# Kernel tuning notes

Hardware: AMD Instinct MI355X
Metric: run time of the kernel (lower is better)

## Reference

```python
import jax, jax.numpy as jnp
import numpy as np

BATCH = 50000      # number of target nodes in the batch (len(to_neighs))
DEGREE = 32        # fixed sampled neighbor count per node
NUM_NODES = 500000 # embedding table size (id2feat domain)
D_FEAT = 128       # feature dim of id2feat


def setup_inputs() -> dict:
    key = jax.random.key(0)
    k1, k2 = jax.random.split(key)
    neighs = jax.random.randint(k1, (BATCH, DEGREE), 0, NUM_NODES, dtype=jnp.int64)
    id2feat_table = jax.random.normal(k2, (NUM_NODES, D_FEAT), dtype=jnp.float32) * 0.02
    return {"neighs": neighs, "id2feat_table": id2feat_table}


def reference(neighs, id2feat_table):
    # Original: mask counts each neighbor occurrence, row-normalized by num_neigh,
    # then mask @ embed_matrix == per-node mean of neighbor embeddings.
    # Fixed degree K, so segment-mean == gather + mean over the neighbor axis.
    neigh_feats = id2feat_table[neighs]        # [B, K, D] gather (memory-bound)
    to_feats = neigh_feats.mean(axis=1)        # [B, D] mean over K neighbors
    return to_feats
```

## Files before the change

kernel.cpp:

```cpp
#include <hip/hip_runtime.h>


constexpr int BATCH  = 50000;
constexpr int DEGREE = 32;
constexpr int D_FEAT = 128;

typedef float f32x4 __attribute__((ext_vector_type(4)));

__global__ __launch_bounds__(256) void MeanAggregator_841813590039_kernel(
    const int* __restrict__ neighs,
    const float* __restrict__ table,
    float* __restrict__ out)
{
    const int wave  = (blockIdx.x * 256 + threadIdx.x) >> 6;
    const int lane  = threadIdx.x & 63;
    const int nodeA = wave * 2;
    const int col   = lane & 31;
    const int half  = lane & 32;

    const int rows = neighs[(size_t)nodeA * DEGREE + lane];

    #define ROW(k) __shfl(rows, half + (k), 64)
    #define LOADK(k) \
        reinterpret_cast<const f32x4*>(table + (size_t)ROW(k) * D_FEAT)[col]

    f32x4 buf0[8], buf1[8];

    #pragma unroll
    for (int j = 0; j < 8; ++j) buf0[j] = LOADK(j);

    f32x4 acc = {0.f, 0.f, 0.f, 0.f};

    #pragma unroll
    for (int g = 0; g < 3; ++g) {
        f32x4* cur = (g & 1) ? buf1 : buf0;
        f32x4* nxt = (g & 1) ? buf0 : buf1;
        #pragma unroll
        for (int j = 0; j < 8; ++j) nxt[j] = LOADK((g + 1) * 8 + j);
        #pragma unroll
        for (int j = 0; j < 8; ++j) acc += cur[j];
    }
    #pragma unroll
    for (int j = 0; j < 8; ++j) acc += buf1[j];

    #undef LOADK
    #undef ROW

    const float inv = 1.0f / (float)DEGREE;
    acc *= inv;

    const int node = nodeA + (half >> 5);
    f32x4* o = reinterpret_cast<f32x4*>(out + (size_t)node * D_FEAT) + col;
    __builtin_nontemporal_store(acc, o);
}

extern "C" void kernel_launch(void* const* d_in, const int* in_sizes, int n_in,
                              void* d_out, int out_size, void* d_ws, size_t ws_size,
                              hipStream_t stream) {
    const int*   neighs = (const int*)d_in[0];
    const float* table  = (const float*)d_in[1];
    float*       out    = (float*)d_out;

    const int grid = BATCH / 8;
    MeanAggregator_841813590039_kernel<<<grid, 256, 0, stream>>>(neighs, table, out);
}
```

Measured before the change: 400.6 us.

## Process eight node pairs per wave with bitonic-sorted neighbor ids

Each wave now handles eight node pairs instead of one, interleaving gathers across pairs with a double-buffered loop over the 32 neighbors. Neighbor ids for each node are bitonic-sorted within the 32-lane half before gathering, so loads issued together touch nearby table rows and may get better cache or TLB locality. The grid shrinks by a factor of eight, and launch bounds are raised to request higher occupancy. The costs are extra shuffle and compare work for the sort, higher register pressure from eight accumulators and buffers, and fewer waves available to hide latency.

```diff
diff --git a/kernel.cpp b/kernel.cpp
--- a/kernel.cpp
+++ b/kernel.cpp
@@ -4,54 +4,87 @@
 constexpr int BATCH  = 50000;
 constexpr int DEGREE = 32;
 constexpr int D_FEAT = 128;
+constexpr int PW     = 8;
+constexpr int NPAIRS = BATCH / 2;
+constexpr int WAVES  = (NPAIRS + PW - 1) / PW;
+constexpr int BLOCKS = (WAVES + 3) / 4;
 
 typedef float f32x4 __attribute__((ext_vector_type(4)));
 
-__global__ __launch_bounds__(256) void MeanAggregator_841813590039_kernel(
+__global__ __launch_bounds__(256, 4) void MeanAggregator_841813590039_kernel(
     const int* __restrict__ neighs,
     const float* __restrict__ table,
     float* __restrict__ out)
 {
-    const int wave  = (blockIdx.x * 256 + threadIdx.x) >> 6;
-    const int lane  = threadIdx.x & 63;
-    const int nodeA = wave * 2;
-    const int col   = lane & 31;
-    const int half  = lane & 32;
+    const int wave = blockIdx.x * 4 + (threadIdx.x >> 6);
+    const int lane = threadIdx.x & 63;
+    const int col  = lane & 31;
+    const int half = lane & 32;
 
-    const int rows = neighs[(size_t)nodeA * DEGREE + lane];
+    if (wave >= WAVES) return;
 
-    #define ROW(k) __shfl(rows, half + (k), 64)
-    #define LOADK(k) \
-        reinterpret_cast<const f32x4*>(table + (size_t)ROW(k) * D_FEAT)[col]
+    const int pair0 = wave * PW;
 
-    f32x4 buf0[8], buf1[8];
+    int rows[PW];
+    #pragma unroll
+    for (int i = 0; i < PW; ++i)
+        rows[i] = neighs[(size_t)(pair0 + i) * (2 * DEGREE) + lane];
 
     #pragma unroll
-    for (int j = 0; j < 8; ++j) buf0[j] = LOADK(j);
+    for (int i = 0; i < PW; ++i) {
+        int v = rows[i];
+        #pragma unroll
+        for (int size = 2; size <= 32; size <<= 1) {
+            #pragma unroll
+            for (int stride = size >> 1; stride > 0; stride >>= 1) {
+                const int  pv    = __shfl_xor(v, stride, 64);
+                const bool up    = ((col & size) == 0);
+                const bool lower = ((col & stride) == 0);
+                const int  mn    = (v < pv) ? v : pv;
+                const int  mx    = (v < pv) ? pv : v;
+                v = (lower == up) ? mn : mx;
+            }
+        }
+        rows[i] = v;
+    }
 
-    f32x4 acc = {0.f, 0.f, 0.f, 0.f};
+    #define LOADKJ(j, k) \
+        reinterpret_cast<const f32x4*>( \
+            table + (size_t)__shfl(rows[(j)], half + (k), 64) * D_FEAT)[col]
+
+    f32x4 acc[PW];
+    #pragma unroll
+    for (int j = 0; j < PW; ++j) acc[j] = f32x4{0.f, 0.f, 0.f, 0.f};
+
+    f32x4 buf0[PW], buf1[PW];
 
     #pragma unroll
-    for (int g = 0; g < 3; ++g) {
-        f32x4* cur = (g & 1) ? buf1 : buf0;
-        f32x4* nxt = (g & 1) ? buf0 : buf1;
+    for (int j = 0; j < PW; ++j) buf0[j] = LOADKJ(j, 0);
+
+    #pragma unroll
+    for (int k = 0; k < DEGREE - 1; ++k) {
+        f32x4* cur = (k & 1) ? buf1 : buf0;
+        f32x4* nxt = (k & 1) ? buf0 : buf1;
         #pragma unroll
-        for (int j = 0; j < 8; ++j) nxt[j] = LOADK((g + 1) * 8 + j);
+        for (int j = 0; j < PW; ++j) nxt[j] = LOADKJ(j, k + 1);
         #pragma unroll
-        for (int j = 0; j < 8; ++j) acc += cur[j];
+        for (int j = 0; j < PW; ++j) acc[j] += cur[j];
     }
     #pragma unroll
-    for (int j = 0; j < 8; ++j) acc += buf1[j];
+    for (int j = 0; j < PW; ++j) acc[j] += buf1[j];
 
-    #undef LOADK
-    #undef ROW
+    #undef LOADKJ
 
     const float inv = 1.0f / (float)DEGREE;
-    acc *= inv;
 
-    const int node = nodeA + (half >> 5);
-    f32x4* o = reinterpret_cast<f32x4*>(out + (size_t)node * D_FEAT) + col;
-    __builtin_nontemporal_store(acc, o);
+    #pragma unroll
+    for (int i = 0; i < PW; ++i) {
+        const int node = (pair0 + i) * 2 + (half >> 5);
+        f32x4 v = acc[i];
+        v *= inv;
+        __builtin_nontemporal_store(
+            v, reinterpret_cast<f32x4*>(out + (size_t)node * D_FEAT) + col);
+    }
 }
 
 extern "C" void kernel_launch(void* const* d_in, const int* in_sizes, int n_in,
@@ -61,6 +94,5 @@
     const float* table  = (const float*)d_in[1];
     float*       out    = (float*)d_out;
 
-    const int grid = BATCH / 8;
-    MeanAggregator_841813590039_kernel<<<grid, 256, 0, stream>>>(neighs, table, out);
+    MeanAggregator_841813590039_kernel<<<BLOCKS, 256, 0, stream>>>(neighs, table, out);
 }
```

Measured after the change: 378.4 us. 1.06x faster.
